# Kernel tuning notes

Measured on AMD Instinct MI355X. Metric: run time of the kernel, lower is better.

## Reference

```python
import math
import jax, jax.numpy as jnp
import numpy as np

D = 512; H = 8; N = 6; DFF = 2048; VS = 32000; VT = 32000
B = 4; S = 1024; T = 1024
EPS = 1e-5


def _pe(length, d):
    pos = jnp.arange(length, dtype=jnp.float32)[:, None]
    div = jnp.exp(jnp.arange(0, d, 2, dtype=jnp.float32) * (-math.log(10000.0) / d))
    pe = jnp.zeros((length, d), jnp.float32)
    pe = pe.at[:, 0::2].set(jnp.sin(pos * div)).at[:, 1::2].set(jnp.cos(pos * div))
    return pe  # [L, D]


def _ln(x, g, b):
    m = x.mean(-1, keepdims=True)
    v = ((x - m) ** 2).mean(-1, keepdims=True)
    return (x - m) / jnp.sqrt(v + EPS) * g + b


def _mha(xq, xkv, w, b, mask):
    # w: [4, D, D], b: [4, D]; mask broadcastable to [B, H, Sq, Sk]
    nb, sq, d = xq.shape
    dk = d // H
    def proj(x, i):
        return (x @ w[i] + b[i]).reshape(x.shape[0], x.shape[1], H, dk).transpose(0, 2, 1, 3)
    q, k, v = proj(xq, 0), proj(xkv, 1), proj(xkv, 2)
    scores = jnp.einsum('bhqd,bhkd->bhqk', q, k) / math.sqrt(dk)
    scores = jnp.where(mask == 0, -1e9, scores)
    p = jax.nn.softmax(scores, axis=-1)
    o = jnp.einsum('bhqk,bhkd->bhqd', p, v).transpose(0, 2, 1, 3).reshape(nb, sq, d)
    return o @ w[3] + b[3]


def _ffn(x, w1, b1, w2, b2):
    return jax.nn.relu(x @ w1 + b1) @ w2 + b2


def _forward(src_emb, tgt_emb,
             enc_attn_w, enc_attn_b, enc_ffn_w1, enc_ffn_b1, enc_ffn_w2, enc_ffn_b2,
             enc_ln_g, enc_ln_b, enc_fg, enc_fb,
             dec_self_w, dec_self_b, dec_src_w, dec_src_b,
             dec_ffn_w1, dec_ffn_b1, dec_ffn_w2, dec_ffn_b2,
             dec_ln_g, dec_ln_b, dec_fg, dec_fb,
             gen_w, gen_b,
             src, tgt, src_mask, tgt_mask):
    # embed + positional encoding (dropout off: eval mode)
    x = src_emb[src] + _pe(src.shape[1], D)[None]
    for i in range(N):
        a = _mha(x, x, enc_attn_w[i], enc_attn_b[i], src_mask)
        x = _ln(x + a, enc_ln_g[i, 0], enc_ln_b[i, 0])
        f = _ffn(x, enc_ffn_w1[i], enc_ffn_b1[i], enc_ffn_w2[i], enc_ffn_b2[i])
        x = _ln(x + f, enc_ln_g[i, 1], enc_ln_b[i, 1])
    memory = _ln(x, enc_fg, enc_fb)

    y = tgt_emb[tgt] + _pe(tgt.shape[1], D)[None]
    for i in range(N):
        a = _mha(y, y, dec_self_w[i], dec_self_b[i], tgt_mask)
        y = _ln(y + a, dec_ln_g[i, 0], dec_ln_b[i, 0])
        a = _mha(y, memory, dec_src_w[i], dec_src_b[i], src_mask)
        y = _ln(y + a, dec_ln_g[i, 1], dec_ln_b[i, 1])
        f = _ffn(y, dec_ffn_w1[i], dec_ffn_b1[i], dec_ffn_w2[i], dec_ffn_b2[i])
        y = _ln(y + f, dec_ln_g[i, 2], dec_ln_b[i, 2])
    y = _ln(y, dec_fg, dec_fb)
    return y @ gen_w + gen_b  # [B, T, VT]


def setup_inputs():
    key = jax.random.key(0)
    ks = iter(jax.random.split(key, 48))
    def w(*shape):
        return jax.random.normal(next(ks), shape, dtype=jnp.float32) * 0.02
    inp = {}
    inp['src_emb'] = w(VS, D)
    inp['tgt_emb'] = w(VT, D)
    inp['enc_attn_w'] = w(N, 4, D, D)
    inp['enc_attn_b'] = jnp.zeros((N, 4, D), jnp.float32)
    inp['enc_ffn_w1'] = w(N, D, DFF)
    inp['enc_ffn_b1'] = jnp.zeros((N, DFF), jnp.float32)
    inp['enc_ffn_w2'] = w(N, DFF, D)
    inp['enc_ffn_b2'] = jnp.zeros((N, D), jnp.float32)
    inp['enc_ln_g'] = jnp.ones((N, 2, D), jnp.float32)
    inp['enc_ln_b'] = jnp.zeros((N, 2, D), jnp.float32)
    inp['enc_fg'] = jnp.ones((D,), jnp.float32)
    inp['enc_fb'] = jnp.zeros((D,), jnp.float32)
    inp['dec_self_w'] = w(N, 4, D, D)
    inp['dec_self_b'] = jnp.zeros((N, 4, D), jnp.float32)
    inp['dec_src_w'] = w(N, 4, D, D)
    inp['dec_src_b'] = jnp.zeros((N, 4, D), jnp.float32)
    inp['dec_ffn_w1'] = w(N, D, DFF)
    inp['dec_ffn_b1'] = jnp.zeros((N, DFF), jnp.float32)
    inp['dec_ffn_w2'] = w(N, DFF, D)
    inp['dec_ffn_b2'] = jnp.zeros((N, D), jnp.float32)
    inp['dec_ln_g'] = jnp.ones((N, 3, D), jnp.float32)
    inp['dec_ln_b'] = jnp.zeros((N, 3, D), jnp.float32)
    inp['dec_fg'] = jnp.ones((D,), jnp.float32)
    inp['dec_fb'] = jnp.zeros((D,), jnp.float32)
    inp['gen_w'] = w(D, VT)
    inp['gen_b'] = jnp.zeros((VT,), jnp.float32)
    inp['src'] = jax.random.randint(next(ks), (B, S), 0, VS)
    inp['tgt'] = jax.random.randint(next(ks), (B, T), 0, VT)
    inp['src_mask'] = jnp.ones((B, 1, 1, S), jnp.int32)
    inp['tgt_mask'] = jnp.tril(jnp.ones((T, T), jnp.int32))[None, None]  # causal [1,1,T,T]
    return inp


def reference(src_emb, tgt_emb, enc_attn_w, enc_attn_b, enc_ffn_w1, enc_ffn_b1,
              enc_ffn_w2, enc_ffn_b2, enc_ln_g, enc_ln_b, enc_fg, enc_fb,
              dec_self_w, dec_self_b, dec_src_w, dec_src_b,
              dec_ffn_w1, dec_ffn_b1, dec_ffn_w2, dec_ffn_b2,
              dec_ln_g, dec_ln_b, dec_fg, dec_fb, gen_w, gen_b,
              src, tgt, src_mask, tgt_mask):
    return _forward(src_emb, tgt_emb, enc_attn_w, enc_attn_b, enc_ffn_w1, enc_ffn_b1,
                    enc_ffn_w2, enc_ffn_b2, enc_ln_g, enc_ln_b, enc_fg, enc_fb,
                    dec_self_w, dec_self_b, dec_src_w, dec_src_b,
                    dec_ffn_w1, dec_ffn_b1, dec_ffn_w2, dec_ffn_b2,
                    dec_ln_g, dec_ln_b, dec_fg, dec_fb, gen_w, gen_b,
                    src, tgt, src_mask, tgt_mask)
```

## Files before the change

### kernel.cpp

```cpp
#include <hip/hip_runtime.h>


typedef __bf16 bf16x8 __attribute__((ext_vector_type(8)));
typedef __bf16 bf16x4 __attribute__((ext_vector_type(4)));
typedef float  f32x4  __attribute__((ext_vector_type(4)));

__device__ __forceinline__ void gload_lds16(const void* g, void* l) {
  __builtin_amdgcn_global_load_lds((__attribute__((address_space(1))) void*)g,
                                   (__attribute__((address_space(3))) void*)l,
                                   16, 0, 0);
}

__device__ __forceinline__ void hard_barrier() {
  asm volatile("" ::: "memory");
  __builtin_amdgcn_sched_barrier(0);
  __builtin_amdgcn_s_barrier();
  __builtin_amdgcn_sched_barrier(0);
  asm volatile("" ::: "memory");
}

template<int EPI>
__global__ __launch_bounds__(256)
void gemm2_kernel(const __bf16* __restrict__ A, const __bf16* __restrict__ Akv,
                  int lda,
                  const __bf16* __restrict__ BT, int ldb,
                  void* __restrict__ Cv, int ldc,
                  const float* __restrict__ bias, int K,
                  __bf16* __restrict__ qb, __bf16* __restrict__ kb,
                  __bf16* __restrict__ vt)
{
  constexpr int BM = 128, BN = 128, BK = 64;
  constexpr int WM = 64, WN = 64, FM = 4, FN = 4;
  constexpr int SLOT = 2 * BM * BK;
  __shared__ char ldsraw[69632];
  __bf16* lds = (__bf16*)ldsraw;
  const int tid  = threadIdx.x;
  const int lane = tid & 63, wave = tid >> 6;
  const int wr = wave >> 1, wc = wave & 1;
  const int bm = blockIdx.x * BM, bn = blockIdx.y * BN;
  const __bf16* Ause = (EPI == 2 && blockIdx.y >= 4) ? Akv : A;

  auto stage = [&](int slot, int kt) {
    const char* Ag = (const char*)Ause;
    const char* Bg = (const char*)BT;
    char* base = (char*)(lds + slot * SLOT);
    const long long k0b = (long long)kt * (BK * 2);
#pragma unroll
    for (int i = 0; i < 4; i++) {
      int t = tid + i * 256;
      int row = t >> 3, cb = (t & 7) << 4;
      int src = cb ^ ((row & 7) << 4);
      gload_lds16(Ag + ((long long)(bm + row) * lda) * 2 + k0b + src, base + t * 16);
    }
#pragma unroll
    for (int i = 0; i < 4; i++) {
      int t = tid + i * 256;
      int row = t >> 3, cb = (t & 7) << 4;
      int src = cb ^ ((row & 7) << 4);
      gload_lds16(Bg + ((long long)(bn + row) * ldb) * 2 + k0b + src,
                  base + BM * BK * 2 + t * 16);
    }
  };

  f32x4 acc[FM][FN] = {};
  const int NT = K / BK;

  stage(0, 0);
  stage(1, 1);

  for (int t = 0; t < NT; t++) {
    if (t < NT - 1) {
      asm volatile("s_waitcnt vmcnt(8)" ::: "memory");
    } else {
      asm volatile("s_waitcnt vmcnt(0)" ::: "memory");
    }
    hard_barrier();
    const char* sA = (const char*)(lds + (t & 1) * SLOT);
    const char* sB = sA + BM * BK * 2;
#pragma unroll
    for (int kk = 0; kk < 2; kk++) {
      const int g = kk * 64 + (lane >> 4) * 16;
      bf16x8 af[FM], bfr[FN];
#pragma unroll
      for (int i = 0; i < FM; i++) {
        int row = wr * WM + i * 16 + (lane & 15);
        af[i] = *(const bf16x8*)(sA + row * 128 + (g ^ ((row & 7) << 4)));
      }
#pragma unroll
      for (int j = 0; j < FN; j++) {
        int row = wc * WN + j * 16 + (lane & 15);
        bfr[j] = *(const bf16x8*)(sB + row * 128 + (g ^ ((row & 7) << 4)));
      }
      __builtin_amdgcn_s_setprio(1);
#pragma unroll
      for (int i = 0; i < FM; i++)
#pragma unroll
        for (int j = 0; j < FN; j++)
          acc[i][j] = __builtin_amdgcn_mfma_f32_16x16x32_bf16(af[i], bfr[j], acc[i][j], 0, 0, 0);
      __builtin_amdgcn_s_setprio(0);
    }
    hard_barrier();
    if (t + 2 < NT) stage(t & 1, t + 2);
  }

  if constexpr (EPI == 3) {
    __syncthreads();
    float* ct = (float*)ldsraw;
#pragma unroll
    for (int i = 0; i < FM; i++) {
#pragma unroll
      for (int j = 0; j < FN; j++) {
        int lrow = wr * WM + i * 16 + (lane >> 4) * 4;
        int lcol = wc * WN + j * 16 + (lane & 15);
        float bv = bias[bn + lcol];
#pragma unroll
        for (int r = 0; r < 4; r++)
          ct[(lrow + r) * 132 + lcol] = acc[i][j][r] + bv;
      }
    }
    __syncthreads();
    float* C = (float*)Cv;
#pragma unroll
    for (int it = 0; it < 16; it++) {
      int idx = tid + it * 256;
      int row = idx >> 5, c4 = (idx & 31) * 4;
      f32x4 v = *(const f32x4*)(ct + row * 132 + c4);
      *(f32x4*)(C + (long long)(bm + row) * ldc + bn + c4) = v;
    }
    return;
  }

#pragma unroll
  for (int i = 0; i < FM; i++) {
#pragma unroll
    for (int j = 0; j < FN; j++) {
      int row0 = bm + wr * WM + i * 16 + (lane >> 4) * 4;
      int col  = bn + wc * WN + j * 16 + (lane & 15);
      float bv = bias ? bias[col] : 0.f;
      if constexpr (EPI == 2) {
        int z = col >> 9;
        int cw = col & 511;
        int b = row0 >> 10, s = row0 & 1023;
        int h = cw >> 6, dk = cw & 63;
        long long bh = b * 8 + h;
        if (z == 2) {
          bf16x4 vv;
#pragma unroll
          for (int r = 0; r < 4; r++) vv[r] = (__bf16)(acc[i][j][r] + bv);
          *(bf16x4*)(vt + (bh << 16) + (dk << 10) + s) = vv;
        } else {
          __bf16* dst = (z == 0) ? qb : kb;
          float sc = (z == 0) ? 0.125f : 1.0f;
#pragma unroll
          for (int r = 0; r < 4; r++)
            dst[(bh << 16) + ((long long)(s + r) << 6) + dk] = (__bf16)((acc[i][j][r] + bv) * sc);
        }
      } else if constexpr (EPI == 1) {
        __bf16* C = (__bf16*)Cv;
#pragma unroll
        for (int r = 0; r < 4; r++)
          C[(long long)(row0 + r) * ldc + col] = (__bf16)fmaxf(acc[i][j][r] + bv, 0.f);
      } else {
        float* C = (float*)Cv;
#pragma unroll
        for (int r = 0; r < 4; r++)
          C[(long long)(row0 + r) * ldc + col] = acc[i][j][r] + bv;
      }
    }
  }
}

__global__ __launch_bounds__(256)
void gemm_kernel(const __bf16* __restrict__ A, int lda,
                 const __bf16* __restrict__ BT, int ldb,
                 float* __restrict__ C, int ldc,
                 const float* __restrict__ bias, int K)
{
  constexpr int BM = 128, BN = 64, BK = 64;
  constexpr int WM = 64, WN = 32, FM = 4, FN = 2;
  constexpr int LA = (BM * BK) / 2048;
  constexpr int LB = (BN * BK) / 2048;
  constexpr int SLOT = (BM + BN) * BK;
  __shared__ __bf16 lds[3 * SLOT];
  const int tid  = threadIdx.x;
  const int lane = tid & 63, wave = tid >> 6;
  const int wr = wave >> 1, wc = wave & 1;
  const int bm = blockIdx.x * BM, bn = blockIdx.y * BN;

  auto stage = [&](int slot, int kt) {
    const char* Ag = (const char*)A;
    const char* Bg = (const char*)BT;
    char* base = (char*)(lds + slot * SLOT);
    const long long k0b = (long long)kt * (BK * 2);
#pragma unroll
    for (int i = 0; i < LA; i++) {
      int t = tid + i * 256;
      int row = t >> 3, cb = (t & 7) << 4;
      int src = cb ^ ((row & 7) << 4);
      gload_lds16(Ag + ((long long)(bm + row) * lda) * 2 + k0b + src, base + t * 16);
    }
#pragma unroll
    for (int i = 0; i < LB; i++) {
      int t = tid + i * 256;
      int row = t >> 3, cb = (t & 7) << 4;
      int src = cb ^ ((row & 7) << 4);
      gload_lds16(Bg + ((long long)(bn + row) * ldb) * 2 + k0b + src,
                  base + BM * BK * 2 + t * 16);
    }
  };

  f32x4 acc[FM][FN] = {};
  const int NT = K / BK;

  stage(0, 0);
  stage(1, 1);

  for (int t = 0; t < NT; t++) {
    if (t < NT - 1) {
      asm volatile("s_waitcnt vmcnt(6)" ::: "memory");
    } else {
      asm volatile("s_waitcnt vmcnt(0)" ::: "memory");
    }
    hard_barrier();
    if (t + 2 < NT) stage((t + 2) % 3, t + 2);
    const char* sA = (const char*)(lds + (t % 3) * SLOT);
    const char* sB = sA + BM * BK * 2;
#pragma unroll
    for (int kk = 0; kk < 2; kk++) {
      const int g = kk * 64 + (lane >> 4) * 16;
      bf16x8 af[FM], bfr[FN];
#pragma unroll
      for (int i = 0; i < FM; i++) {
        int row = wr * WM + i * 16 + (lane & 15);
        af[i] = *(const bf16x8*)(sA + row * 128 + (g ^ ((row & 7) << 4)));
      }
#pragma unroll
      for (int j = 0; j < FN; j++) {
        int row = wc * WN + j * 16 + (lane & 15);
        bfr[j] = *(const bf16x8*)(sB + row * 128 + (g ^ ((row & 7) << 4)));
      }
      __builtin_amdgcn_s_setprio(1);
#pragma unroll
      for (int i = 0; i < FM; i++)
#pragma unroll
        for (int j = 0; j < FN; j++)
          acc[i][j] = __builtin_amdgcn_mfma_f32_16x16x32_bf16(af[i], bfr[j], acc[i][j], 0, 0, 0);
      __builtin_amdgcn_s_setprio(0);
    }
  }

#pragma unroll
  for (int i = 0; i < FM; i++) {
#pragma unroll
    for (int j = 0; j < FN; j++) {
      int row0 = bm + wr * WM + i * 16 + (lane >> 4) * 4;
      int col  = bn + wc * WN + j * 16 + (lane & 15);
      float bv = bias ? bias[col] : 0.f;
#pragma unroll
      for (int r = 0; r < 4; r++)
        C[(long long)(row0 + r) * ldc + col] = acc[i][j][r] + bv;
    }
  }
}

template<int CAUSAL>
__global__ __launch_bounds__(256)
void flash_kernel(const __bf16* __restrict__ qb, const __bf16* __restrict__ kb,
                  const __bf16* __restrict__ vt, const int* __restrict__ smask,
                  __bf16* __restrict__ Ob)
{
  __shared__ __bf16 lK[2 * 128 * 64];
  __shared__ __bf16 lV[2 * 64 * 128];
  __shared__ __bf16 lP[4][16 * 128];
  const int bh = blockIdx.y;
  const int b = bh >> 3, h = bh & 7;
  const int q0 = blockIdx.x * 64;
  const int tid = threadIdx.x, lane = tid & 63, w = tid >> 6;
  const char* kh = (const char*)(kb + ((long long)bh << 16));
  const char* vh = (const char*)(vt + ((long long)bh << 16));

  auto stageKV = [&](int buf, int t) {
    int k0 = t * 128;
#pragma unroll
    for (int i = 0; i < 4; i++) {
      int c = tid + i * 256;
      int row = c >> 3, cb = (c & 7) << 4;
      int cl = cb ^ ((row & 7) << 4);
      gload_lds16(kh + (long long)(k0 + row) * 128 + cl, (char*)lK + buf * 16384 + c * 16);
    }
#pragma unroll
    for (int i = 0; i < 4; i++) {
      int c = tid + i * 256;
      int row = c >> 4, cb = (c & 15) << 4;
      int cl = cb ^ ((row & 7) << 4);
      gload_lds16(vh + (long long)row * 2048 + (long long)k0 * 2 + cl, (char*)lV + buf * 16384 + c * 16);
    }
  };

  bf16x8 qa[2];
  {
    const __bf16* qrow = qb + ((long long)bh << 16)
                       + (long long)(q0 + w * 16 + (lane & 15)) * 64 + (lane >> 4) * 8;
    qa[0] = *(const bf16x8*)(qrow);
    qa[1] = *(const bf16x8*)(qrow + 32);
  }
  f32x4 oacc[4] = {};
  float m[4], l[4];
#pragma unroll
  for (int r = 0; r < 4; r++) { m[r] = -3e38f; l[r] = 0.f; }

  const int nt = CAUSAL ? (blockIdx.x / 2 + 1) : 8;
  char* lPw = (char*)lP + w * 4096;

  stageKV(0, 0);
  if (nt > 1) stageKV(1, 1);

  for (int t = 0; t < nt; t++) {
    const int k0 = t * 128;
    if (t < nt - 1) {
      asm volatile("s_waitcnt vmcnt(8)" ::: "memory");
    } else {
      asm volatile("s_waitcnt vmcnt(0)" ::: "memory");
    }
    hard_barrier();
    char* cK = (char*)lK + (t & 1) * 16384;
    char* cV = (char*)lV + (t & 1) * 16384;

    f32x4 sf[8];
#pragma unroll
    for (int f = 0; f < 8; f++) {
      int row = f * 16 + (lane & 15);
      f32x4 s = {};
#pragma unroll
      for (int ks = 0; ks < 2; ks++) {
        int cb = ks * 64 + (lane >> 4) * 16;
        bf16x8 kf = *(const bf16x8*)(cK + row * 128 + (cb ^ ((row & 7) << 4)));
        s = __builtin_amdgcn_mfma_f32_16x16x32_bf16(qa[ks], kf, s, 0, 0, 0);
      }
      sf[f] = s;
    }

    if (!CAUSAL) {
#pragma unroll
      for (int f = 0; f < 8; f++) {
        if (smask[b * 1024 + k0 + f * 16 + (lane & 15)] == 0) {
#pragma unroll
          for (int r = 0; r < 4; r++) sf[f][r] = -1e30f;
        }
      }
    } else if (t == nt - 1) {
#pragma unroll
      for (int f = 0; f < 8; f++) {
        int kc = k0 + f * 16 + (lane & 15);
#pragma unroll
        for (int r = 0; r < 4; r++) {
          int qr = q0 + w * 16 + (lane >> 4) * 4 + r;
          if (kc > qr) sf[f][r] = -1e30f;
        }
      }
    }

    float mt[4];
#pragma unroll
    for (int r = 0; r < 4; r++) {
      float v = sf[0][r];
#pragma unroll
      for (int f = 1; f < 8; f++) v = fmaxf(v, sf[f][r]);
      mt[r] = v;
    }
#pragma unroll
    for (int o = 1; o < 16; o <<= 1)
#pragma unroll
      for (int r = 0; r < 4; r++) mt[r] = fmaxf(mt[r], __shfl_xor(mt[r], o));

    bool need = false;
#pragma unroll
    for (int r = 0; r < 4; r++) need = need || (mt[r] > m[r] + 8.f);
    if (__any(need)) {
      float mn[4], cr[4];
#pragma unroll
      for (int r = 0; r < 4; r++) {
        mn[r] = fmaxf(m[r], mt[r]);
        cr[r] = __expf(m[r] - mn[r]);
        m[r]  = mn[r];
        l[r] *= cr[r];
      }
#pragma unroll
      for (int d = 0; d < 4; d++)
#pragma unroll
        for (int r = 0; r < 4; r++) oacc[d][r] *= cr[r];
    }
    float rs[4] = {0.f, 0.f, 0.f, 0.f};
#pragma unroll
    for (int f = 0; f < 8; f++)
#pragma unroll
      for (int r = 0; r < 4; r++) {
        float p = __expf(sf[f][r] - m[r]);
        sf[f][r] = p;
        rs[r] += p;
      }
#pragma unroll
    for (int o = 1; o < 16; o <<= 1)
#pragma unroll
      for (int r = 0; r < 4; r++) rs[r] += __shfl_xor(rs[r], o);
#pragma unroll
    for (int r = 0; r < 4; r++) l[r] += rs[r];

#pragma unroll
    for (int f = 0; f < 8; f++) {
      int colB = f * 32 + (lane & 15) * 2;
#pragma unroll
      for (int r = 0; r < 4; r++) {
        int row = (lane >> 4) * 4 + r;
        *(__bf16*)(lPw + row * 256 + (colB ^ ((row & 7) << 4))) = (__bf16)sf[f][r];
      }
    }
    asm volatile("s_waitcnt lgkmcnt(0)" ::: "memory");

#pragma unroll
    for (int ks = 0; ks < 4; ks++) {
      int prow = lane & 15;
      int cb = ks * 64 + (lane >> 4) * 16;
      bf16x8 pa = *(const bf16x8*)(lPw + prow * 256 + (cb ^ ((prow & 7) << 4)));
#pragma unroll
      for (int d = 0; d < 4; d++) {
        int vrow = d * 16 + (lane & 15);
        bf16x8 vf = *(const bf16x8*)(cV + vrow * 256 + (cb ^ ((vrow & 7) << 4)));
        oacc[d] = __builtin_amdgcn_mfma_f32_16x16x32_bf16(pa, vf, oacc[d], 0, 0, 0);
      }
    }
    hard_barrier();
    if (t + 2 < nt) stageKV(t & 1, t + 2);
  }

  float inv[4];
#pragma unroll
  for (int r = 0; r < 4; r++) inv[r] = 1.f / l[r];
#pragma unroll
  for (int d = 0; d < 4; d++)
#pragma unroll
    for (int r = 0; r < 4; r++) {
      long long row = b * 1024 + q0 + w * 16 + (lane >> 4) * 4 + r;
      Ob[row * 512 + h * 64 + d * 16 + (lane & 15)] = (__bf16)(oacc[d][r] * inv[r]);
    }
}

__global__ void transpose_w_kernel(const float* __restrict__ W, __bf16* __restrict__ WT,
                                   int K, int N)
{
  __shared__ float t[32][33];
  long long mz = (long long)blockIdx.z * K * N;
  W += mz; WT += mz;
  int n0 = blockIdx.x * 32, k0 = blockIdx.y * 32;
  int tx = threadIdx.x, ty = threadIdx.y;
#pragma unroll
  for (int i = 0; i < 32; i += 8)
    t[ty + i][tx] = W[(long long)(k0 + ty + i) * N + (n0 + tx)];
  __syncthreads();
#pragma unroll
  for (int i = 0; i < 32; i += 8)
    WT[(long long)(n0 + ty + i) * K + (k0 + tx)] = (__bf16)t[tx][ty + i];
}

__global__ void embed_kernel(const float* __restrict__ emb, const int* __restrict__ idx,
                             __bf16* __restrict__ Xb)
{
  int row = blockIdx.x;
  int s   = row & 1023;
  int tok = idx[row];
  int d0  = threadIdx.x * 4;
  float4 e = *(const float4*)(emb + (long long)tok * 512 + d0);
  const float* ep = (const float*)&e;
  bf16x4 ob;
#pragma unroll
  for (int j = 0; j < 4; j++) {
    int d = d0 + j;
    float div = expf((float)(d & ~1) * (-9.210340371976184f / 512.f));
    float ang = (float)s * div;
    float pe  = (d & 1) ? cosf(ang) : sinf(ang);
    ob[j] = (__bf16)(ep[j] + pe);
  }
  *(bf16x4*)(Xb + (long long)row * 512 + d0) = ob;
}

__global__ void ln_kernel(const __bf16* __restrict__ Xin, const float* __restrict__ Rin,
                          const float* __restrict__ g, const float* __restrict__ b,
                          __bf16* __restrict__ Xbout)
{
  int row = blockIdx.x, lane = threadIdx.x;
  long long base = (long long)row * 512 + lane * 8;
  bf16x8 xv = *(const bf16x8*)(Xin + base);
  float x[8];
#pragma unroll
  for (int i = 0; i < 8; i++) x[i] = (float)xv[i];
  if (Rin) {
    float4 r0 = *(const float4*)(Rin + base);
    float4 r1 = *(const float4*)(Rin + base + 4);
    x[0] += r0.x; x[1] += r0.y; x[2] += r0.z; x[3] += r0.w;
    x[4] += r1.x; x[5] += r1.y; x[6] += r1.z; x[7] += r1.w;
  }
  float s = 0.f;
#pragma unroll
  for (int i = 0; i < 8; i++) s += x[i];
#pragma unroll
  for (int o = 32; o > 0; o >>= 1) s += __shfl_xor(s, o);
  float mean = s * (1.f / 512.f);
  float v = 0.f;
#pragma unroll
  for (int i = 0; i < 8; i++) { x[i] -= mean; v += x[i] * x[i]; }
#pragma unroll
  for (int o = 32; o > 0; o >>= 1) v += __shfl_xor(v, o);
  float inv = rsqrtf(v * (1.f / 512.f) + 1e-5f);
  int d0 = lane * 8;
  float gg[8], bb[8];
  *(float4*)gg       = *(const float4*)(g + d0);
  *(float4*)(gg + 4) = *(const float4*)(g + d0 + 4);
  *(float4*)bb       = *(const float4*)(b + d0);
  *(float4*)(bb + 4) = *(const float4*)(b + d0 + 4);
  bf16x8 yb;
#pragma unroll
  for (int i = 0; i < 8; i++)
    yb[i] = (__bf16)(x[i] * inv * gg[i] + bb[i]);
  *(bf16x8*)(Xbout + base) = yb;
}

extern "C" void kernel_launch(void* const* d_in, const int* in_sizes, int n_in,
                              void* d_out, int out_size, void* d_ws, size_t ws_size,
                              hipStream_t stream)
{
  (void)in_sizes; (void)n_in; (void)out_size; (void)ws_size;
  const float* src_emb    = (const float*)d_in[0];
  const float* tgt_emb    = (const float*)d_in[1];
  const float* enc_attn_w = (const float*)d_in[2];
  const float* enc_attn_b = (const float*)d_in[3];
  const float* enc_ffn_w1 = (const float*)d_in[4];
  const float* enc_ffn_b1 = (const float*)d_in[5];
  const float* enc_ffn_w2 = (const float*)d_in[6];
  const float* enc_ffn_b2 = (const float*)d_in[7];
  const float* enc_ln_g   = (const float*)d_in[8];
  const float* enc_ln_b   = (const float*)d_in[9];
  const float* enc_fg     = (const float*)d_in[10];
  const float* enc_fb     = (const float*)d_in[11];
  const float* dec_self_w = (const float*)d_in[12];
  const float* dec_self_b = (const float*)d_in[13];
  const float* dec_src_w  = (const float*)d_in[14];
  const float* dec_src_b  = (const float*)d_in[15];
  const float* dec_ffn_w1 = (const float*)d_in[16];
  const float* dec_ffn_b1 = (const float*)d_in[17];
  const float* dec_ffn_w2 = (const float*)d_in[18];
  const float* dec_ffn_b2 = (const float*)d_in[19];
  const float* dec_ln_g   = (const float*)d_in[20];
  const float* dec_ln_b   = (const float*)d_in[21];
  const float* dec_fg     = (const float*)d_in[22];
  const float* dec_fb     = (const float*)d_in[23];
  const float* gen_w      = (const float*)d_in[24];
  const float* gen_b      = (const float*)d_in[25];
  const int*   src        = (const int*)d_in[26];
  const int*   tgt        = (const int*)d_in[27];
  const int*   src_mask   = (const int*)d_in[28];

  float* out = (float*)d_out;

  char* wp = (char*)d_ws;
  auto alloc = [&](size_t bytes) { void* p = (void*)wp; wp += (bytes + 255) & ~(size_t)255; return p; };
  __bf16* TWea = (__bf16*)alloc(24ull * 262144 * 2);
  __bf16* TWe1 = (__bf16*)alloc(6ull * 1048576 * 2);
  __bf16* TWe2 = (__bf16*)alloc(6ull * 1048576 * 2);
  __bf16* TWds = (__bf16*)alloc(24ull * 262144 * 2);
  __bf16* TWdx = (__bf16*)alloc(24ull * 262144 * 2);
  __bf16* TWd1 = (__bf16*)alloc(6ull * 1048576 * 2);
  __bf16* TWd2 = (__bf16*)alloc(6ull * 1048576 * 2);
  __bf16* Xb   = (__bf16*)alloc(4096ull * 512 * 2);
  __bf16* MEMb = (__bf16*)alloc(4096ull * 512 * 2);
  float*  R    = (float*) alloc(4096ull * 512 * 4);
  __bf16* qb   = (__bf16*)alloc(32ull * 1024 * 64 * 2);
  __bf16* kb   = (__bf16*)alloc(32ull * 1024 * 64 * 2);
  __bf16* vt   = (__bf16*)alloc(32ull * 1024 * 64 * 2);
  __bf16* Ob   = (__bf16*)alloc(4096ull * 512 * 2);
  __bf16* Fb   = qb;
  __bf16* GENT = TWea;

  transpose_w_kernel<<<dim3(16, 16, 24), dim3(32, 8), 0, stream>>>(enc_attn_w, TWea, 512, 512);
  transpose_w_kernel<<<dim3(64, 16, 6),  dim3(32, 8), 0, stream>>>(enc_ffn_w1, TWe1, 512, 2048);
  transpose_w_kernel<<<dim3(16, 64, 6),  dim3(32, 8), 0, stream>>>(enc_ffn_w2, TWe2, 2048, 512);
  transpose_w_kernel<<<dim3(16, 16, 24), dim3(32, 8), 0, stream>>>(dec_self_w, TWds, 512, 512);
  transpose_w_kernel<<<dim3(16, 16, 24), dim3(32, 8), 0, stream>>>(dec_src_w,  TWdx, 512, 512);
  transpose_w_kernel<<<dim3(64, 16, 6),  dim3(32, 8), 0, stream>>>(dec_ffn_w1, TWd1, 512, 2048);
  transpose_w_kernel<<<dim3(16, 64, 6),  dim3(32, 8), 0, stream>>>(dec_ffn_w2, TWd2, 2048, 512);

  auto attention = [&](const __bf16* wt, const float* bptr, int causal,
                       const __bf16* Aq, const __bf16* Akv) {
    gemm2_kernel<2><<<dim3(32, 12), 256, 0, stream>>>(
        Aq, Akv, 512, wt, 512, nullptr, 0, bptr, 512, qb, kb, vt);
    if (causal)
      flash_kernel<1><<<dim3(16, 32), 256, 0, stream>>>(qb, kb, vt, nullptr, Ob);
    else
      flash_kernel<0><<<dim3(16, 32), 256, 0, stream>>>(qb, kb, vt, src_mask, Ob);
    gemm_kernel<<<dim3(32, 8), 256, 0, stream>>>(
        Ob, 512, wt + 3 * 262144, 512, R, 512, bptr + 3 * 512, 512);
  };

  auto ffn = [&](const __bf16* w1t, const float* b1, const __bf16* w2t, const float* b2) {
    gemm2_kernel<1><<<dim3(32, 16), 256, 0, stream>>>(
        Xb, Xb, 512, w1t, 512, Fb, 2048, b1, 512, nullptr, nullptr, nullptr);
    gemm_kernel<<<dim3(32, 8), 256, 0, stream>>>(
        Fb, 2048, w2t, 2048, R, 512, b2, 2048);
  };

  embed_kernel<<<4096, 128, 0, stream>>>(src_emb, src, Xb);
  for (int i = 0; i < 6; i++) {
    attention(TWea + (long long)i * 1048576, enc_attn_b + i * 2048, 0, Xb, Xb);
    ln_kernel<<<4096, 64, 0, stream>>>(Xb, R, enc_ln_g + i * 1024, enc_ln_b + i * 1024, Xb);
    ffn(TWe1 + (long long)i * 1048576, enc_ffn_b1 + i * 2048,
        TWe2 + (long long)i * 1048576, enc_ffn_b2 + i * 512);
    ln_kernel<<<4096, 64, 0, stream>>>(Xb, R, enc_ln_g + i * 1024 + 512, enc_ln_b + i * 1024 + 512, Xb);
  }
  ln_kernel<<<4096, 64, 0, stream>>>(Xb, nullptr, enc_fg, enc_fb, MEMb);

  transpose_w_kernel<<<dim3(1000, 16, 1), dim3(32, 8), 0, stream>>>(gen_w, GENT, 512, 32000);

  embed_kernel<<<4096, 128, 0, stream>>>(tgt_emb, tgt, Xb);
  for (int i = 0; i < 6; i++) {
    attention(TWds + (long long)i * 1048576, dec_self_b + i * 2048, 1, Xb, Xb);
    ln_kernel<<<4096, 64, 0, stream>>>(Xb, R, dec_ln_g + i * 1536, dec_ln_b + i * 1536, Xb);

    attention(TWdx + (long long)i * 1048576, dec_src_b + i * 2048, 0, Xb, MEMb);
    ln_kernel<<<4096, 64, 0, stream>>>(Xb, R, dec_ln_g + i * 1536 + 512, dec_ln_b + i * 1536 + 512, Xb);

    ffn(TWd1 + (long long)i * 1048576, dec_ffn_b1 + i * 2048,
        TWd2 + (long long)i * 1048576, dec_ffn_b2 + i * 512);
    ln_kernel<<<4096, 64, 0, stream>>>(Xb, R, dec_ln_g + i * 1536 + 1024, dec_ln_b + i * 1536 + 1024, Xb);
  }
  ln_kernel<<<4096, 64, 0, stream>>>(Xb, nullptr, dec_fg, dec_fb, Xb);

  gemm2_kernel<3><<<dim3(32, 250), 256, 0, stream>>>(
      Xb, Xb, 512, GENT, 512, out, 32000, gen_b, 512, nullptr, nullptr, nullptr);
}
```

Measured before the change: 1.843 ms.

## Use 256x256-tile 512-thread GEMM kernel for the vocabulary generator projection

Adds a dedicated GEMM kernel with 256x256 output tiles, 8 waves and 128KB of LDS double buffering for the final 4096x32000x512 generator projection. It replaces the 128x128-tile EPI==3 path, and the epilogue is staged through LDS in four 64-row chunks. Larger tiles raise arithmetic intensity and cut how often A and B are re-read, in exchange for more LDS and registers per workgroup, lower occupancy, and an extra barrier inside each k-step. The old kernel's LDS array shrinks to 64KB now that its f32 epilogue staging is gone.

```diff
diff --git a/kernel.cpp b/kernel.cpp
--- a/kernel.cpp
+++ b/kernel.cpp
@@ -17,6 +17,125 @@
   __builtin_amdgcn_s_barrier();
   __builtin_amdgcn_sched_barrier(0);
   asm volatile("" ::: "memory");
+}
+
+__global__ __launch_bounds__(512, 2)
+void gemm256_kernel(const __bf16* __restrict__ A, int lda,
+                    const __bf16* __restrict__ BT, int ldb,
+                    float* __restrict__ C, int ldc,
+                    const float* __restrict__ bias, int K)
+{
+  __shared__ char ldsraw[131072];
+  const int tid  = threadIdx.x;
+  const int lane = tid & 63, wid = tid >> 6;
+  const int wr = wid >> 2, wc = wid & 3;
+  const int bm = blockIdx.x * 256, bn = blockIdx.y * 256;
+
+  auto stage = [&](int slot, int kt) {
+    const char* Ag = (const char*)A;
+    const char* Bg = (const char*)BT;
+    char* base = ldsraw + slot * 65536;
+    const long long k0b = (long long)kt * 128;
+#pragma unroll
+    for (int i = 0; i < 4; i++) {
+      int t = tid + i * 512;
+      int row = t >> 3, cb = (t & 7) << 4;
+      int src = cb ^ ((row & 7) << 4);
+      gload_lds16(Ag + ((long long)(bm + row) * lda) * 2 + k0b + src, base + t * 16);
+    }
+#pragma unroll
+    for (int i = 0; i < 4; i++) {
+      int t = tid + i * 512;
+      int row = t >> 3, cb = (t & 7) << 4;
+      int src = cb ^ ((row & 7) << 4);
+      gload_lds16(Bg + ((long long)(bn + row) * ldb) * 2 + k0b + src,
+                  base + 32768 + t * 16);
+    }
+  };
+
+  f32x4 acc[8][4] = {};
+  const int NT = K / 64;
+
+  stage(0, 0);
+  stage(1, 1);
+
+  for (int kt = 0; kt < NT; kt++) {
+    if (kt < NT - 1) {
+      asm volatile("s_waitcnt vmcnt(8)" ::: "memory");
+    } else {
+      asm volatile("s_waitcnt vmcnt(0)" ::: "memory");
+    }
+    hard_barrier();
+    const char* sA = ldsraw + (kt & 1) * 65536;
+    const char* sB = sA + 32768;
+#pragma unroll
+    for (int q = 0; q < 4; q++) {
+      const int qr = q >> 1, qc = q & 1;
+      bf16x8 af[4][2], bf[2][2];
+#pragma unroll
+      for (int i = 0; i < 4; i++) {
+        int row = wr * 128 + (qr * 4 + i) * 16 + (lane & 15);
+#pragma unroll
+        for (int kk = 0; kk < 2; kk++) {
+          int g = kk * 64 + (lane >> 4) * 16;
+          af[i][kk] = *(const bf16x8*)(sA + row * 128 + (g ^ ((row & 7) << 4)));
+        }
+      }
+#pragma unroll
+      for (int j = 0; j < 2; j++) {
+        int row = wc * 64 + (qc * 2 + j) * 16 + (lane & 15);
+#pragma unroll
+        for (int kk = 0; kk < 2; kk++) {
+          int g = kk * 64 + (lane >> 4) * 16;
+          bf[j][kk] = *(const bf16x8*)(sB + row * 128 + (g ^ ((row & 7) << 4)));
+        }
+      }
+      __builtin_amdgcn_s_barrier();
+      asm volatile("s_waitcnt lgkmcnt(0)" ::: "memory");
+      __builtin_amdgcn_sched_barrier(0);
+      __builtin_amdgcn_s_setprio(1);
+#pragma unroll
+      for (int kk = 0; kk < 2; kk++)
+#pragma unroll
+        for (int i = 0; i < 4; i++)
+#pragma unroll
+          for (int j = 0; j < 2; j++)
+            acc[qr * 4 + i][qc * 2 + j] = __builtin_amdgcn_mfma_f32_16x16x32_bf16(
+                af[i][kk], bf[j][kk], acc[qr * 4 + i][qc * 2 + j], 0, 0, 0);
+      __builtin_amdgcn_s_setprio(0);
+    }
+    hard_barrier();
+    if (kt + 2 < NT) stage(kt & 1, kt + 2);
+  }
+
+  float* ct = (float*)ldsraw;
+#pragma unroll
+  for (int c = 0; c < 4; c++) {
+    __syncthreads();
+    if (wr == (c >> 1)) {
+      const int ib = (c & 1) * 4;
+#pragma unroll
+      for (int i = 0; i < 4; i++) {
+#pragma unroll
+        for (int j = 0; j < 4; j++) {
+          int lrow = i * 16 + (lane >> 4) * 4;
+          int lcol = wc * 64 + j * 16 + (lane & 15);
+          float bv = bias[bn + lcol];
+#pragma unroll
+          for (int r = 0; r < 4; r++)
+            ct[(lrow + r) * 260 + lcol] = acc[ib + i][j][r] + bv;
+        }
+      }
+    }
+    __syncthreads();
+#pragma unroll
+    for (int it = 0; it < 8; it++) {
+      int idx = tid + it * 512;
+      int row = idx >> 6, c4 = (idx & 63) * 4;
+      f32x4 v = *(const f32x4*)(ct + row * 260 + c4);
+      *(f32x4*)(C + (long long)(bm + c * 64 + row) * ldc + bn + c4) = v;
+    }
+  }
 }
 
 template<int EPI>
@@ -32,7 +151,7 @@
   constexpr int BM = 128, BN = 128, BK = 64;
   constexpr int WM = 64, WN = 64, FM = 4, FN = 4;
   constexpr int SLOT = 2 * BM * BK;
-  __shared__ char ldsraw[69632];
+  __shared__ char ldsraw[65536];
   __bf16* lds = (__bf16*)ldsraw;
   const int tid  = threadIdx.x;
   const int lane = tid & 63, wave = tid >> 6;
@@ -101,33 +220,6 @@
     }
     hard_barrier();
     if (t + 2 < NT) stage(t & 1, t + 2);
-  }
-
-  if constexpr (EPI == 3) {
-    __syncthreads();
-    float* ct = (float*)ldsraw;
-#pragma unroll
-    for (int i = 0; i < FM; i++) {
-#pragma unroll
-      for (int j = 0; j < FN; j++) {
-        int lrow = wr * WM + i * 16 + (lane >> 4) * 4;
-        int lcol = wc * WN + j * 16 + (lane & 15);
-        float bv = bias[bn + lcol];
-#pragma unroll
-        for (int r = 0; r < 4; r++)
-          ct[(lrow + r) * 132 + lcol] = acc[i][j][r] + bv;
-      }
-    }
-    __syncthreads();
-    float* C = (float*)Cv;
-#pragma unroll
-    for (int it = 0; it < 16; it++) {
-      int idx = tid + it * 256;
-      int row = idx >> 5, c4 = (idx & 31) * 4;
-      f32x4 v = *(const f32x4*)(ct + row * 132 + c4);
-      *(f32x4*)(C + (long long)(bm + row) * ldc + bn + c4) = v;
-    }
-    return;
   }
 
 #pragma unroll
@@ -633,6 +725,6 @@
   }
   ln_kernel<<<4096, 64, 0, stream>>>(Xb, nullptr, dec_fg, dec_fb, Xb);
 
-  gemm2_kernel<3><<<dim3(32, 250), 256, 0, stream>>>(
-      Xb, Xb, 512, GENT, 512, out, 32000, gen_b, 512, nullptr, nullptr, nullptr);
-}
+  gemm256_kernel<<<dim3(16, 125), 512, 0, stream>>>(
+      Xb, 512, GENT, 512, out, 32000, gen_b, 512);
+}
```

New measurement: 1.836 ms. No clear change (-0.3%).
